# Performance work log

Measured on AMD Instinct MI355X. Metric: run time of the kernel, lower is better.

Reference implementation:

```python
import jax, jax.numpy as jnp
import numpy as np

D_MODEL = 1024
N_HEAD = 16


def setup_inputs() -> dict:
    key = jax.random.key(0)
    ks = jax.random.split(key, 12)
    B, T, D = 2, 2048, D_MODEL
    s = 1.0 / np.sqrt(D)
    return {
        "q": jax.random.normal(ks[0], (B, T, D), jnp.float32),
        "k": jax.random.normal(ks[1], (B, T, D), jnp.float32),
        "v": jax.random.normal(ks[2], (B, T, D), jnp.float32),
        "w_q": jax.random.normal(ks[3], (D, D), jnp.float32) * s,
        "b_q": jnp.zeros((D,), jnp.float32),
        "w_k": jax.random.normal(ks[4], (D, D), jnp.float32) * s,
        "b_k": jnp.zeros((D,), jnp.float32),
        "w_v": jax.random.normal(ks[5], (D, D), jnp.float32) * s,
        "b_v": jnp.zeros((D,), jnp.float32),
        "w_o": jax.random.normal(ks[6], (D, D), jnp.float32) * s,
        "b_o": jnp.zeros((D,), jnp.float32),
    }


def reference(q, k, v, w_q, b_q, w_k, b_k, w_v, b_v, w_o, b_o):
    B, T, D = q.shape
    H = N_HEAD
    nd = D // H  # head dim
    # projections (weights stored as [in, out])
    qh = (q @ w_q + b_q).reshape(B, T, H, nd).transpose(0, 2, 1, 3)  # [b,h,t,nd]
    kh = (k @ w_k + b_k).reshape(B, T, H, nd).transpose(0, 2, 1, 3)
    vh = (v @ w_v + b_v).reshape(B, T, H, nd).transpose(0, 2, 1, 3)
    score = jnp.einsum('bhqd,bhkd->bhqk', qh, kh) / jnp.sqrt(jnp.float32(nd))
    causal = jnp.tril(jnp.ones((T, T), dtype=bool))  # [tq, tk]
    score = jnp.where(causal, score, -jnp.inf)
    # NOTE: original module uses nn.Softmax(dim=-2), i.e. softmax over the
    # QUERY axis. Faithful to the source.
    attn = jax.nn.softmax(score, axis=-2)
    out = jnp.einsum('bhqk,bhkd->bhqd', attn, vh)  # [b,h,t,nd]
    out = out.transpose(0, 2, 1, 3).reshape(B, T, D)
    return out @ w_o + b_o
```

## Files before the change

### kernel.cpp

```cpp
#include <hip/hip_runtime.h>
#include <hip/hip_bf16.h>
#include <cstdint>
#include <cstddef>

#define D_MODEL 1024
#define NHEAD   16
#define HDIM    64
#define BB      2
#define TT      2048
#define MM      (BB*TT)
#define BHN     (BB*NHEAD)

typedef __attribute__((ext_vector_type(8))) __bf16 bf16x8;
typedef __attribute__((ext_vector_type(4))) float  f32x4;
typedef __attribute__((ext_vector_type(8))) unsigned short u16x8;
typedef __attribute__((ext_vector_type(4))) unsigned short u16x4;

__device__ __forceinline__ unsigned short f2b(float f){
  __bf16 b = (__bf16)f;
  return __builtin_bit_cast(unsigned short, b);
}
__device__ __forceinline__ float b2f(unsigned short u){
  unsigned int x = ((unsigned int)u) << 16;
  return __builtin_bit_cast(float, x);
}

__device__ __forceinline__ f32x4 mfma16(bf16x8 a, bf16x8 b, f32x4 c){
  return __builtin_amdgcn_mfma_f32_16x16x32_bf16(a, b, c, 0, 0, 0);
}

__device__ __forceinline__ void gload16(const void* g, void* lds){
  __builtin_amdgcn_global_load_lds((const __attribute__((address_space(1))) void*)g,
                                   (__attribute__((address_space(3))) void*)lds, 16, 0, 0);
}

__global__ void cvt_bf16_kernel(const float* __restrict__ q, const float* __restrict__ k,
                                const float* __restrict__ v,
                                unsigned short* __restrict__ Xq, unsigned short* __restrict__ Xk,
                                unsigned short* __restrict__ Xv){
  const int z = blockIdx.y;
  const float* x = z==0 ? q : z==1 ? k : v;
  unsigned short* y = z==0 ? Xq : z==1 ? Xk : Xv;
  size_t i = (size_t)blockIdx.x*blockDim.x + threadIdx.x;
  const float4* p = (const float4*)(x + i*8);
  float4 a = p[0], b = p[1];
  u16x8 o;
  o[0]=f2b(a.x); o[1]=f2b(a.y); o[2]=f2b(a.z); o[3]=f2b(a.w);
  o[4]=f2b(b.x); o[5]=f2b(b.y); o[6]=f2b(b.z); o[7]=f2b(b.w);
  *(u16x8*)(y + i*8) = o;
}

__global__ void transpose_w_kernel(const float* __restrict__ W0, const float* __restrict__ W1,
                                   const float* __restrict__ W2, const float* __restrict__ W3,
                                   unsigned short* __restrict__ T0, unsigned short* __restrict__ T1,
                                   unsigned short* __restrict__ T2, unsigned short* __restrict__ T3){
  __shared__ float tile[32][33];
  const int z = blockIdx.z;
  const float* W = z==0 ? W0 : z==1 ? W1 : z==2 ? W2 : W3;
  unsigned short* Wt = z==0 ? T0 : z==1 ? T1 : z==2 ? T2 : T3;
  int tx = threadIdx.x, ty = threadIdx.y;
  int x0 = blockIdx.x*32, y0 = blockIdx.y*32;
  #pragma unroll
  for (int i=0;i<4;i++)
    tile[ty + i*8][tx] = W[(size_t)(y0 + ty + i*8)*D_MODEL + x0 + tx];
  __syncthreads();
  #pragma unroll
  for (int i=0;i<4;i++)
    Wt[(size_t)(x0 + ty + i*8)*D_MODEL + y0 + tx] = f2b(tile[tx][ty + i*8]);
}

__device__ __forceinline__ void gemm_body(const unsigned short* __restrict__ A,
                                          const unsigned short* __restrict__ Bt,
                                          const float* __restrict__ bias,
                                          void* __restrict__ Cout, const int mode,
                                          const int m0, const int n0)
{
  constexpr int K = D_MODEL, N = D_MODEL;
  __shared__ unsigned short As[2][128*32];
  __shared__ unsigned short Bs[2][128*32];
  const int t = threadIdx.x, lane = t&63, w = t>>6;
  const int wr = w>>1, wc = w&1, lr = lane&15, lg = lane>>4;
  const int srow = lane>>2;
  const int schunk = (lane&3) ^ ((lane>>3)&3);
  const int crd = lg ^ ((lr>>1)&3);
  f32x4 acc[4][4] = {};

  auto stage = [&](int buf, int k0){
    #pragma unroll
    for (int g=0; g<2; g++){
      int reg = w*2 + g;
      int r = reg*16 + srow;
      gload16(A  + (size_t)(m0+r)*K + k0 + schunk*8, (char*)As[buf] + reg*1024);
      gload16(Bt + (size_t)(n0+r)*K + k0 + schunk*8, (char*)Bs[buf] + reg*1024);
    }
  };

  stage(0, 0);
  __syncthreads();
  int buf = 0;
  for (int ks = 0; ks < 32; ++ks){
    if (ks < 31) stage(buf^1, (ks+1)*32);
    const char* bufA = (const char*)As[buf];
    const char* bufB = (const char*)Bs[buf];
    bf16x8 af[4], bfv[4];
    #pragma unroll
    for (int mi=0;mi<4;mi++){
      int r = wr*64 + mi*16 + lr;
      af[mi] = *(const bf16x8*)(bufA + r*64 + crd*16);
    }
    #pragma unroll
    for (int ni=0;ni<4;ni++){
      int r = wc*64 + ni*16 + lr;
      bfv[ni] = *(const bf16x8*)(bufB + r*64 + crd*16);
    }
    #pragma unroll
    for (int mi=0;mi<4;mi++)
      #pragma unroll
      for (int ni=0;ni<4;ni++)
        acc[mi][ni] = mfma16(af[mi], bfv[ni], acc[mi][ni]);
    __syncthreads();
    buf ^= 1;
  }

  #pragma unroll
  for (int mi=0;mi<4;mi++){
    #pragma unroll
    for (int ni=0;ni<4;ni++){
      int n = n0 + wc*64 + ni*16 + lr;
      int mbase = m0 + wr*64 + mi*16 + lg*4;
      float bv = bias[n];
      if (mode == 0){
        unsigned short* Cb = (unsigned short*)Cout;
        #pragma unroll
        for (int r=0;r<4;r++) Cb[(size_t)(mbase+r)*N + n] = f2b(acc[mi][ni][r] + bv);
      } else {
        unsigned short* Vt = (unsigned short*)Cout;
        int h = n >> 6, d = n & 63;
        int b = mbase >> 11;
        int tq = mbase & (TT-1);
        u16x4 vv;
        #pragma unroll
        for (int r=0;r<4;r++) vv[r] = f2b(acc[mi][ni][r] + bv);
        *(u16x4*)(Vt + ((size_t)((b*NHEAD + h)*HDIM + d))*TT + tq) = vv;
      }
    }
  }
}

__launch_bounds__(256)
__global__ void proj_gemm_kernel(const unsigned short* __restrict__ Xq,
                                 const unsigned short* __restrict__ Xk,
                                 const unsigned short* __restrict__ Xv,
                                 const unsigned short* __restrict__ Wtq,
                                 const unsigned short* __restrict__ Wtk,
                                 const unsigned short* __restrict__ Wtv,
                                 const float* __restrict__ b_q, const float* __restrict__ b_k,
                                 const float* __restrict__ b_v,
                                 unsigned short* __restrict__ Qb, unsigned short* __restrict__ Kb,
                                 unsigned short* __restrict__ Vt)
{
  const int id = blockIdx.x;
  const int xcd = id & 7, r2 = id >> 3;
  const int n = r2 & 7, mz = r2 >> 3;
  const int m = (mz & 3)*8 + xcd, z = mz >> 2;
  const unsigned short* A  = z==0 ? Xq : z==1 ? Xk : Xv;
  const unsigned short* Bt = z==0 ? Wtq : z==1 ? Wtk : Wtv;
  const float* bias = z==0 ? b_q : z==1 ? b_k : b_v;
  void* C = z==0 ? (void*)Qb : z==1 ? (void*)Kb : (void*)Vt;
  gemm_body(A, Bt, bias, C, z==2 ? 1 : 0, m*128, n*128);
}

__launch_bounds__(256)
__global__ void out_gemm_kernel(const unsigned short* __restrict__ Ob,
                                const unsigned short* __restrict__ Wto,
                                const float* __restrict__ b_o, float* __restrict__ out)
{
  constexpr int K = D_MODEL, N = D_MODEL;
  __shared__ unsigned short As[2][64*32];
  __shared__ unsigned short Bs[2][128*32];
  const int id = blockIdx.x;
  const int xcd = id & 7, r2 = id >> 3;
  const int n0 = (r2 & 7)*128, m0 = ((r2 >> 3)*8 + xcd)*64;
  const int t = threadIdx.x, lane = t&63, w = t>>6;
  const int wr = w>>1, wc = w&1, lr = lane&15, lg = lane>>4;
  const int srow = lane>>2;
  const int schunk = (lane&3) ^ ((lane>>3)&3);
  const int crd = lg ^ ((lr>>1)&3);
  f32x4 acc[2][4] = {};

  auto stage = [&](int buf, int k0){
    { int r = w*16 + srow;
      gload16(Ob + (size_t)(m0+r)*K + k0 + schunk*8, (char*)As[buf] + w*1024); }
    #pragma unroll
    for (int g=0; g<2; g++){
      int reg = w*2 + g;
      int r = reg*16 + srow;
      gload16(Wto + (size_t)(n0+r)*K + k0 + schunk*8, (char*)Bs[buf] + reg*1024);
    }
  };

  stage(0, 0);
  __syncthreads();
  int buf = 0;
  for (int ks = 0; ks < 32; ++ks){
    if (ks < 31) stage(buf^1, (ks+1)*32);
    const char* bufA = (const char*)As[buf];
    const char* bufB = (const char*)Bs[buf];
    bf16x8 af[2], bfv[4];
    #pragma unroll
    for (int mi=0;mi<2;mi++){
      int r = wr*32 + mi*16 + lr;
      af[mi] = *(const bf16x8*)(bufA + r*64 + crd*16);
    }
    #pragma unroll
    for (int ni=0;ni<4;ni++){
      int r = wc*64 + ni*16 + lr;
      bfv[ni] = *(const bf16x8*)(bufB + r*64 + crd*16);
    }
    #pragma unroll
    for (int mi=0;mi<2;mi++)
      #pragma unroll
      for (int ni=0;ni<4;ni++)
        acc[mi][ni] = mfma16(af[mi], bfv[ni], acc[mi][ni]);
    __syncthreads();
    buf ^= 1;
  }

  #pragma unroll
  for (int mi=0;mi<2;mi++){
    #pragma unroll
    for (int ni=0;ni<4;ni++){
      int n = n0 + wc*64 + ni*16 + lr;
      int mbase = m0 + wr*32 + mi*16 + lg*4;
      float bv = b_o[n];
      #pragma unroll
      for (int r=0;r<4;r++) out[(size_t)(mbase+r)*N + n] = acc[mi][ni][r] + bv;
    }
  }
}

__launch_bounds__(256)
__global__ void col_stats_kernel(const unsigned short* __restrict__ Qb,
                                 const unsigned short* __restrict__ Kb,
                                 float* __restrict__ partialS)
{
  __shared__ unsigned short Ks[128*64];
  __shared__ unsigned short Qs[2][64*64];
  const int t = threadIdx.x, lane = t&63, w = t>>6;
  const int id = blockIdx.x;
  const int bh = id & 31, pair = id >> 5;
  const int kb_ = pair & 15, qc = pair >> 4;
  const int b = bh >> 4, h = bh & 15;
  const int k0 = kb_ * 128;
  const int lr = lane&15, lg = lane>>4;
  const int osrc = (lane&7) ^ (lane>>3);

  auto stageQ = [&](int buf, int qt){
    #pragma unroll
    for (int g=0; g<2; g++){
      int reg = w*2 + g;
      int r = reg*8 + (lane>>3);
      gload16(Qb + ((size_t)(b*TT + qt + r))*D_MODEL + h*64 + osrc*8,
              (char*)Qs[buf] + reg*1024);
    }
  };

  const int qstart = (k0 > qc*256) ? k0 : qc*256;
  const int qend   = (qc+1)*256;

  #pragma unroll
  for (int g=0; g<4; g++){
    int reg = w*4 + g;
    int r = reg*8 + (lane>>3);
    gload16(Kb + ((size_t)(b*TT + k0 + r))*D_MODEL + h*64 + osrc*8, (char*)Ks + reg*1024);
  }
  if (qstart < qend) stageQ(0, qstart);
  __syncthreads();

  bf16x8 bk[2][2];
  #pragma unroll
  for (int kb=0;kb<2;kb++)
    #pragma unroll
    for (int ks=0;ks<2;ks++){
      int r = w*32 + kb*16 + lr;
      bk[kb][ks] = *(const bf16x8*)((const char*)Ks + r*128 + (((ks*4+lg) ^ (r&7))*16));
    }
  f32x4 sacc[2] = {};
  int buf = 0;
  for (int qt = qstart; qt < qend; qt += 64){
    if (qt + 64 < qend) stageQ(buf^1, qt+64);
    const char* bufQ = (const char*)Qs[buf];
    const bool interior = (qt >= k0 + 128);
    #pragma unroll
    for (int qb=0;qb<4;qb++){
      bf16x8 aq[2];
      #pragma unroll
      for (int ks=0;ks<2;ks++){
        int r = qb*16 + lr;
        aq[ks] = *(const bf16x8*)(bufQ + r*128 + (((ks*4+lg) ^ (r&7))*16));
      }
      f32x4 sf[2] = {};
      #pragma unroll
      for (int ks=0;ks<2;ks++)
        #pragma unroll
        for (int kb=0;kb<2;kb++)
          sf[kb] = mfma16(aq[ks], bk[kb][ks], sf[kb]);
      #pragma unroll
      for (int kb=0;kb<2;kb++){
        int col = k0 + w*32 + kb*16 + lr;
        #pragma unroll
        for (int r=0;r<4;r++){
          float e = __expf(sf[kb][r] * 0.125f);
          if (!interior){
            int qg = qt + qb*16 + lg*4 + r;
            e = (qg >= col) ? e : 0.f;
          }
          sacc[kb][r] += e;
        }
      }
    }
    __syncthreads();
    buf ^= 1;
  }
  #pragma unroll
  for (int kb=0;kb<2;kb++){
    float s = sacc[kb][0] + sacc[kb][1] + sacc[kb][2] + sacc[kb][3];
    s += __shfl_xor(s, 16);
    s += __shfl_xor(s, 32);
    if (lg == 0){
      int col = k0 + w*32 + kb*16 + lr;
      partialS[((size_t)qc*BHN + bh)*TT + col] = s;
    }
  }
}

__global__ void col_combine_kernel(const float* __restrict__ partialS, float* __restrict__ colS){
  int i = blockIdx.x*256 + threadIdx.x;
  float s = 0.f;
  #pragma unroll
  for (int qc=0;qc<8;qc++) s += partialS[(size_t)qc*BHN*TT + i];
  colS[i] = 1.0f / s;
}

__global__ void vscale_kernel(unsigned short* __restrict__ Vt, const float* __restrict__ colS){
  size_t c = (size_t)blockIdx.x*256 + threadIdx.x;
  int t0  = (int)(c & 255) * 8;
  int row = (int)(c >> 8);
  int bh  = row >> 6;
  u16x8 v = *(u16x8*)(Vt + (size_t)row*TT + t0);
  const float4* cs = (const float4*)(colS + (size_t)bh*TT + t0);
  float4 s0 = cs[0], s1 = cs[1];
  v[0]=f2b(b2f(v[0])*s0.x); v[1]=f2b(b2f(v[1])*s0.y);
  v[2]=f2b(b2f(v[2])*s0.z); v[3]=f2b(b2f(v[3])*s0.w);
  v[4]=f2b(b2f(v[4])*s1.x); v[5]=f2b(b2f(v[5])*s1.y);
  v[6]=f2b(b2f(v[6])*s1.z); v[7]=f2b(b2f(v[7])*s1.w);
  *(u16x8*)(Vt + (size_t)row*TT + t0) = v;
}

__launch_bounds__(256)
__global__ void attn_out_kernel(const unsigned short* __restrict__ Qb,
                                const unsigned short* __restrict__ Kb,
                                const unsigned short* __restrict__ Vt,
                                unsigned short* __restrict__ O)
{
  __shared__ unsigned short Qs[64*64];
  __shared__ unsigned short Ks2[2][64*64];
  __shared__ unsigned short Vs[2][64*64];
  __shared__ unsigned short Ps[64*64];
  const int t = threadIdx.x, lane=t&63, w=t>>6;
  const int id = blockIdx.x;
  const int bh = id & 31;
  const int qi = 31 - (id >> 5);
  const int b = bh>>4, h = bh&15;
  const int q0 = qi*64;
  const int lr = lane&15, lg = lane>>4;
  const int osrc = (lane&7) ^ (lane>>3);

  auto stageKV = [&](int buf, int k0){
    #pragma unroll
    for (int g=0; g<2; g++){
      int reg = w*2 + g;
      int r = reg*8 + (lane>>3);
      gload16(Kb + ((size_t)(b*TT + k0 + r))*D_MODEL + h*64 + osrc*8,
              (char*)Ks2[buf] + reg*1024);
      gload16(Vt + ((size_t)(bh*HDIM + r))*TT + k0 + osrc*8,
              (char*)Vs[buf] + reg*1024);
    }
  };

  #pragma unroll
  for (int g=0; g<2; g++){
    int reg = w*2 + g;
    int r = reg*8 + (lane>>3);
    gload16(Qb + ((size_t)(b*TT + q0 + r))*D_MODEL + h*64 + osrc*8, (char*)Qs + reg*1024);
  }
  stageKV(0, 0);
  __syncthreads();

  bf16x8 aq[2];
  #pragma unroll
  for (int ks=0;ks<2;ks++){
    int r = w*16 + lr;
    aq[ks] = *(const bf16x8*)((const char*)Qs + r*128 + (((ks*4+lg) ^ (r&7))*16));
  }
  f32x4 oacc[4] = {};
  const int nkt = qi + 1;
  int buf = 0;
  for (int kt=0; kt<nkt; kt++){
    int k0 = kt*64;
    if (kt+1 < nkt) stageKV(buf^1, k0+64);
    const char* bufK = (const char*)Ks2[buf];
    const char* bufV = (const char*)Vs[buf];
    f32x4 sf[4] = {};
    #pragma unroll
    for (int ks=0;ks<2;ks++)
      #pragma unroll
      for (int kb=0;kb<4;kb++){
        int r = kb*16 + lr;
        bf16x8 bk = *(const bf16x8*)(bufK + r*128 + (((ks*4+lg) ^ (r&7))*16));
        sf[kb] = mfma16(bk, aq[ks], sf[kb]);
      }
    const bool boundary = (kt == qi);
    const int prow = w*16 + lr;
    #pragma unroll
    for (int kb=0;kb<4;kb++){
      u16x4 vv;
      #pragma unroll
      for (int r=0;r<4;r++){
        float pv = __expf(sf[kb][r]*0.125f);
        if (boundary){
          int kg = k0 + kb*16 + lg*4 + r;
          int qg = q0 + prow;
          pv = (qg >= kg) ? pv : 0.f;
        }
        vv[r] = f2b(pv);
      }
      *(u16x4*)((char*)Ps + ((prow*128 + kb*32 + lg*8) ^ ((prow&7)<<4))) = vv;
    }
    #pragma unroll
    for (int ks=0;ks<2;ks++){
      bf16x8 pa = *(const bf16x8*)((const char*)Ps + prow*128 + (((ks*4+lg) ^ (prow&7))*16));
      #pragma unroll
      for (int db=0;db<4;db++){
        int r = db*16 + lr;
        bf16x8 bv = *(const bf16x8*)(bufV + r*128 + (((ks*4+lg) ^ (r&7))*16));
        oacc[db] = mfma16(pa, bv, oacc[db]);
      }
    }
    __syncthreads();
    buf ^= 1;
  }
  #pragma unroll
  for (int db=0;db<4;db++){
    int qg = q0 + w*16 + lg*4;
    int d  = db*16 + lr;
    #pragma unroll
    for (int r=0;r<4;r++)
      O[((size_t)(b*TT + qg + r))*D_MODEL + h*64 + d] = f2b(oacc[db][r]);
  }
}

extern "C" void kernel_launch(void* const* d_in, const int* in_sizes, int n_in,
                              void* d_out, int out_size, void* d_ws, size_t ws_size,
                              hipStream_t stream)
{
  (void)in_sizes; (void)n_in; (void)out_size; (void)ws_size;
  const float* q   = (const float*)d_in[0];
  const float* k   = (const float*)d_in[1];
  const float* v   = (const float*)d_in[2];
  const float* w_q = (const float*)d_in[3];
  const float* b_q = (const float*)d_in[4];
  const float* w_k = (const float*)d_in[5];
  const float* b_k = (const float*)d_in[6];
  const float* w_v = (const float*)d_in[7];
  const float* b_v = (const float*)d_in[8];
  const float* w_o = (const float*)d_in[9];
  const float* b_o = (const float*)d_in[10];

  char* p = (char*)d_ws;
  auto carve = [&](size_t bytes)->char* {
    char* r = p; p += (bytes + 255) & ~(size_t)255; return r;
  };
  unsigned short* Xq  = (unsigned short*)carve((size_t)MM*D_MODEL*2);
  unsigned short* Xk  = (unsigned short*)carve((size_t)MM*D_MODEL*2);
  unsigned short* Xv  = (unsigned short*)carve((size_t)MM*D_MODEL*2);
  unsigned short* Wtq = (unsigned short*)carve((size_t)D_MODEL*D_MODEL*2);
  unsigned short* Wtk = (unsigned short*)carve((size_t)D_MODEL*D_MODEL*2);
  unsigned short* Wtv = (unsigned short*)carve((size_t)D_MODEL*D_MODEL*2);
  unsigned short* Wto = (unsigned short*)carve((size_t)D_MODEL*D_MODEL*2);
  unsigned short* Qb  = (unsigned short*)carve((size_t)MM*D_MODEL*2);
  unsigned short* Kb  = (unsigned short*)carve((size_t)MM*D_MODEL*2);
  unsigned short* Vt  = (unsigned short*)carve((size_t)MM*D_MODEL*2);
  unsigned short* Ob  = (unsigned short*)carve((size_t)MM*D_MODEL*2);
  float* partialS = (float*)carve((size_t)8*BHN*TT*4);
  float* colS     = (float*)carve((size_t)BHN*TT*4);

  cvt_bf16_kernel<<<dim3((MM*D_MODEL/8)/256, 3), 256, 0, stream>>>(q, k, v, Xq, Xk, Xv);

  dim3 tgrid(32,32,4), tblk(32,8);
  transpose_w_kernel<<<tgrid, tblk, 0, stream>>>(w_q, w_k, w_v, w_o, Wtq, Wtk, Wtv, Wto);

  proj_gemm_kernel<<<dim3(768), 256, 0, stream>>>(Xq, Xk, Xv, Wtq, Wtk, Wtv,
                                                  b_q, b_k, b_v, Qb, Kb, Vt);

  col_stats_kernel<<<dim3(8*16*BHN), 256, 0, stream>>>(Qb, Kb, partialS);
  col_combine_kernel<<<dim3(BHN*TT/256), 256, 0, stream>>>(partialS, colS);

  vscale_kernel<<<dim3((BHN*HDIM*TT/8)/256), 256, 0, stream>>>(Vt, colS);

  attn_out_kernel<<<dim3((TT/64)*BHN), 256, 0, stream>>>(Qb, Kb, Vt, Ob);

  out_gemm_kernel<<<dim3(512), 256, 0, stream>>>(Ob, Wto, b_o, (float*)d_out);
}
```

Baseline: 140.7 us.

## Fuse input bf16 conversion into projection GEMM, merge colsum with V scaling, enlarge attention tiles

The projection GEMM now reads fp32 q/k/v directly, converts them to bf16 in registers and writes them to LDS. This removes the separate conversion kernel and its bf16 intermediate buffers. The column-sum combine and the V scaling are merged into one kernel. The attention-output kernel now uses 128-query tiles with 512 threads and per-wave causal skipping plus setprio hints. The A-operand loads go through registers rather than async global-to-LDS copies, which adds register pressure and may hurt load/compute overlap.

```diff
diff --git a/kernel.cpp b/kernel.cpp
--- a/kernel.cpp
+++ b/kernel.cpp
@@ -32,22 +32,6 @@
 __device__ __forceinline__ void gload16(const void* g, void* lds){
   __builtin_amdgcn_global_load_lds((const __attribute__((address_space(1))) void*)g,
                                    (__attribute__((address_space(3))) void*)lds, 16, 0, 0);
-}
-
-__global__ void cvt_bf16_kernel(const float* __restrict__ q, const float* __restrict__ k,
-                                const float* __restrict__ v,
-                                unsigned short* __restrict__ Xq, unsigned short* __restrict__ Xk,
-                                unsigned short* __restrict__ Xv){
-  const int z = blockIdx.y;
-  const float* x = z==0 ? q : z==1 ? k : v;
-  unsigned short* y = z==0 ? Xq : z==1 ? Xk : Xv;
-  size_t i = (size_t)blockIdx.x*blockDim.x + threadIdx.x;
-  const float4* p = (const float4*)(x + i*8);
-  float4 a = p[0], b = p[1];
-  u16x8 o;
-  o[0]=f2b(a.x); o[1]=f2b(a.y); o[2]=f2b(a.z); o[3]=f2b(a.w);
-  o[4]=f2b(b.x); o[5]=f2b(b.y); o[6]=f2b(b.z); o[7]=f2b(b.w);
-  *(u16x8*)(y + i*8) = o;
 }
 
 __global__ void transpose_w_kernel(const float* __restrict__ W0, const float* __restrict__ W1,
@@ -69,11 +53,11 @@
     Wt[(size_t)(x0 + ty + i*8)*D_MODEL + y0 + tx] = f2b(tile[tx][ty + i*8]);
 }
 
-__device__ __forceinline__ void gemm_body(const unsigned short* __restrict__ A,
-                                          const unsigned short* __restrict__ Bt,
-                                          const float* __restrict__ bias,
-                                          void* __restrict__ Cout, const int mode,
-                                          const int m0, const int n0)
+__device__ __forceinline__ void gemm_body_f32A(const float* __restrict__ A,
+                                               const unsigned short* __restrict__ Bt,
+                                               const float* __restrict__ bias,
+                                               void* __restrict__ Cout, const int mode,
+                                               const int m0, const int n0)
 {
   constexpr int K = D_MODEL, N = D_MODEL;
   __shared__ unsigned short As[2][128*32];
@@ -82,24 +66,40 @@
   const int wr = w>>1, wc = w&1, lr = lane&15, lg = lane>>4;
   const int srow = lane>>2;
   const int schunk = (lane&3) ^ ((lane>>3)&3);
+  const int ra = t>>1, half = t&1;
+  const int u0 = (half*2)     ^ ((ra>>1)&3);
+  const int u1 = (half*2 + 1) ^ ((ra>>1)&3);
   const int crd = lg ^ ((lr>>1)&3);
   f32x4 acc[4][4] = {};
-
-  auto stage = [&](int buf, int k0){
+  float4 a0,a1,a2,a3;
+
+  auto loadA = [&](int k0){
+    const float4* pa = (const float4*)(A + (size_t)(m0+ra)*K + k0 + half*16);
+    a0=pa[0]; a1=pa[1]; a2=pa[2]; a3=pa[3];
+  };
+  auto writeA = [&](int buf){
+    u16x8 p0, p1;
+    p0[0]=f2b(a0.x); p0[1]=f2b(a0.y); p0[2]=f2b(a0.z); p0[3]=f2b(a0.w);
+    p0[4]=f2b(a1.x); p0[5]=f2b(a1.y); p0[6]=f2b(a1.z); p0[7]=f2b(a1.w);
+    p1[0]=f2b(a2.x); p1[1]=f2b(a2.y); p1[2]=f2b(a2.z); p1[3]=f2b(a2.w);
+    p1[4]=f2b(a3.x); p1[5]=f2b(a3.y); p1[6]=f2b(a3.z); p1[7]=f2b(a3.w);
+    *(u16x8*)((char*)As[buf] + ra*64 + u0*16) = p0;
+    *(u16x8*)((char*)As[buf] + ra*64 + u1*16) = p1;
+  };
+  auto stageB = [&](int buf, int k0){
     #pragma unroll
     for (int g=0; g<2; g++){
       int reg = w*2 + g;
       int r = reg*16 + srow;
-      gload16(A  + (size_t)(m0+r)*K + k0 + schunk*8, (char*)As[buf] + reg*1024);
       gload16(Bt + (size_t)(n0+r)*K + k0 + schunk*8, (char*)Bs[buf] + reg*1024);
     }
   };
 
-  stage(0, 0);
+  loadA(0); stageB(0, 0); writeA(0);
   __syncthreads();
   int buf = 0;
   for (int ks = 0; ks < 32; ++ks){
-    if (ks < 31) stage(buf^1, (ks+1)*32);
+    if (ks < 31){ loadA((ks+1)*32); stageB(buf^1, (ks+1)*32); }
     const char* bufA = (const char*)As[buf];
     const char* bufB = (const char*)Bs[buf];
     bf16x8 af[4], bfv[4];
@@ -118,6 +118,7 @@
       #pragma unroll
       for (int ni=0;ni<4;ni++)
         acc[mi][ni] = mfma16(af[mi], bfv[ni], acc[mi][ni]);
+    if (ks < 31) writeA(buf^1);
     __syncthreads();
     buf ^= 1;
   }
@@ -148,9 +149,9 @@
 }
 
 __launch_bounds__(256)
-__global__ void proj_gemm_kernel(const unsigned short* __restrict__ Xq,
-                                 const unsigned short* __restrict__ Xk,
-                                 const unsigned short* __restrict__ Xv,
+__global__ void proj_gemm_kernel(const float* __restrict__ q,
+                                 const float* __restrict__ k,
+                                 const float* __restrict__ v,
                                  const unsigned short* __restrict__ Wtq,
                                  const unsigned short* __restrict__ Wtk,
                                  const unsigned short* __restrict__ Wtv,
@@ -163,11 +164,11 @@
   const int xcd = id & 7, r2 = id >> 3;
   const int n = r2 & 7, mz = r2 >> 3;
   const int m = (mz & 3)*8 + xcd, z = mz >> 2;
-  const unsigned short* A  = z==0 ? Xq : z==1 ? Xk : Xv;
+  const float* A  = z==0 ? q : z==1 ? k : v;
   const unsigned short* Bt = z==0 ? Wtq : z==1 ? Wtk : Wtv;
   const float* bias = z==0 ? b_q : z==1 ? b_k : b_v;
   void* C = z==0 ? (void*)Qb : z==1 ? (void*)Kb : (void*)Vt;
-  gemm_body(A, Bt, bias, C, z==2 ? 1 : 0, m*128, n*128);
+  gemm_body_f32A(A, Bt, bias, C, z==2 ? 1 : 0, m*128, n*128);
 }
 
 __launch_bounds__(256)
@@ -334,58 +335,46 @@
   }
 }
 
-__global__ void col_combine_kernel(const float* __restrict__ partialS, float* __restrict__ colS){
-  int i = blockIdx.x*256 + threadIdx.x;
+__global__ void col_combine_vscale_kernel(const float* __restrict__ partialS,
+                                          unsigned short* __restrict__ Vt){
+  const int bh = blockIdx.x >> 3, tc = blockIdx.x & 7;
+  const int col = tc*256 + threadIdx.x;
   float s = 0.f;
   #pragma unroll
-  for (int qc=0;qc<8;qc++) s += partialS[(size_t)qc*BHN*TT + i];
-  colS[i] = 1.0f / s;
-}
-
-__global__ void vscale_kernel(unsigned short* __restrict__ Vt, const float* __restrict__ colS){
-  size_t c = (size_t)blockIdx.x*256 + threadIdx.x;
-  int t0  = (int)(c & 255) * 8;
-  int row = (int)(c >> 8);
-  int bh  = row >> 6;
-  u16x8 v = *(u16x8*)(Vt + (size_t)row*TT + t0);
-  const float4* cs = (const float4*)(colS + (size_t)bh*TT + t0);
-  float4 s0 = cs[0], s1 = cs[1];
-  v[0]=f2b(b2f(v[0])*s0.x); v[1]=f2b(b2f(v[1])*s0.y);
-  v[2]=f2b(b2f(v[2])*s0.z); v[3]=f2b(b2f(v[3])*s0.w);
-  v[4]=f2b(b2f(v[4])*s1.x); v[5]=f2b(b2f(v[5])*s1.y);
-  v[6]=f2b(b2f(v[6])*s1.z); v[7]=f2b(b2f(v[7])*s1.w);
-  *(u16x8*)(Vt + (size_t)row*TT + t0) = v;
-}
-
-__launch_bounds__(256)
+  for (int qc=0;qc<8;qc++) s += partialS[((size_t)qc*BHN + bh)*TT + col];
+  const float inv = 1.0f / s;
+  #pragma unroll 8
+  for (int d=0; d<HDIM; d++){
+    size_t idx = ((size_t)(bh*HDIM + d))*TT + col;
+    Vt[idx] = f2b(b2f(Vt[idx]) * inv);
+  }
+}
+
+__launch_bounds__(512)
 __global__ void attn_out_kernel(const unsigned short* __restrict__ Qb,
                                 const unsigned short* __restrict__ Kb,
                                 const unsigned short* __restrict__ Vt,
                                 unsigned short* __restrict__ O)
 {
-  __shared__ unsigned short Qs[64*64];
+  __shared__ unsigned short Qs[128*64];
   __shared__ unsigned short Ks2[2][64*64];
   __shared__ unsigned short Vs[2][64*64];
-  __shared__ unsigned short Ps[64*64];
+  __shared__ unsigned short Ps[128*64];
   const int t = threadIdx.x, lane=t&63, w=t>>6;
   const int id = blockIdx.x;
   const int bh = id & 31;
-  const int qi = 31 - (id >> 5);
+  const int qi = 15 - (id >> 5);
   const int b = bh>>4, h = bh&15;
-  const int q0 = qi*64;
+  const int q0 = qi*128;
   const int lr = lane&15, lg = lane>>4;
   const int osrc = (lane&7) ^ (lane>>3);
 
   auto stageKV = [&](int buf, int k0){
-    #pragma unroll
-    for (int g=0; g<2; g++){
-      int reg = w*2 + g;
-      int r = reg*8 + (lane>>3);
-      gload16(Kb + ((size_t)(b*TT + k0 + r))*D_MODEL + h*64 + osrc*8,
-              (char*)Ks2[buf] + reg*1024);
-      gload16(Vt + ((size_t)(bh*HDIM + r))*TT + k0 + osrc*8,
-              (char*)Vs[buf] + reg*1024);
-    }
+    int r = w*8 + (lane>>3);
+    gload16(Kb + ((size_t)(b*TT + k0 + r))*D_MODEL + h*64 + osrc*8,
+            (char*)Ks2[buf] + w*1024);
+    gload16(Vt + ((size_t)(bh*HDIM + r))*TT + k0 + osrc*8,
+            (char*)Vs[buf] + w*1024);
   };
 
   #pragma unroll
@@ -404,48 +393,55 @@
     aq[ks] = *(const bf16x8*)((const char*)Qs + r*128 + (((ks*4+lg) ^ (r&7))*16));
   }
   f32x4 oacc[4] = {};
-  const int nkt = qi + 1;
+  const int nkt = 2*qi + 2;
   int buf = 0;
   for (int kt=0; kt<nkt; kt++){
     int k0 = kt*64;
     if (kt+1 < nkt) stageKV(buf^1, k0+64);
-    const char* bufK = (const char*)Ks2[buf];
-    const char* bufV = (const char*)Vs[buf];
-    f32x4 sf[4] = {};
-    #pragma unroll
-    for (int ks=0;ks<2;ks++)
+    const bool active = (k0 <= q0 + w*16 + 15);
+    if (active){
+      const char* bufK = (const char*)Ks2[buf];
+      const char* bufV = (const char*)Vs[buf];
+      f32x4 sf[4] = {};
+      __builtin_amdgcn_s_setprio(1);
+      #pragma unroll
+      for (int ks=0;ks<2;ks++)
+        #pragma unroll
+        for (int kb=0;kb<4;kb++){
+          int r = kb*16 + lr;
+          bf16x8 bk = *(const bf16x8*)(bufK + r*128 + (((ks*4+lg) ^ (r&7))*16));
+          sf[kb] = mfma16(bk, aq[ks], sf[kb]);
+        }
+      __builtin_amdgcn_s_setprio(0);
+      const bool boundary = (k0 + 64 > q0 + w*16);
+      const int prow = w*16 + lr;
       #pragma unroll
       for (int kb=0;kb<4;kb++){
-        int r = kb*16 + lr;
-        bf16x8 bk = *(const bf16x8*)(bufK + r*128 + (((ks*4+lg) ^ (r&7))*16));
-        sf[kb] = mfma16(bk, aq[ks], sf[kb]);
+        u16x4 vv;
+        #pragma unroll
+        for (int r=0;r<4;r++){
+          float pv = __expf(sf[kb][r]*0.125f);
+          if (boundary){
+            int kg = k0 + kb*16 + lg*4 + r;
+            int qg = q0 + prow;
+            pv = (qg >= kg) ? pv : 0.f;
+          }
+          vv[r] = f2b(pv);
+        }
+        *(u16x4*)((char*)Ps + ((prow*128 + kb*32 + lg*8) ^ ((prow&7)<<4))) = vv;
       }
-    const bool boundary = (kt == qi);
-    const int prow = w*16 + lr;
-    #pragma unroll
-    for (int kb=0;kb<4;kb++){
-      u16x4 vv;
-      #pragma unroll
-      for (int r=0;r<4;r++){
-        float pv = __expf(sf[kb][r]*0.125f);
-        if (boundary){
-          int kg = k0 + kb*16 + lg*4 + r;
-          int qg = q0 + prow;
-          pv = (qg >= kg) ? pv : 0.f;
+      __builtin_amdgcn_s_setprio(1);
+      #pragma unroll
+      for (int ks=0;ks<2;ks++){
+        bf16x8 pa = *(const bf16x8*)((const char*)Ps + prow*128 + (((ks*4+lg) ^ (prow&7))*16));
+        #pragma unroll
+        for (int db=0;db<4;db++){
+          int r = db*16 + lr;
+          bf16x8 bv = *(const bf16x8*)(bufV + r*128 + (((ks*4+lg) ^ (r&7))*16));
+          oacc[db] = mfma16(pa, bv, oacc[db]);
         }
-        vv[r] = f2b(pv);
       }
-      *(u16x4*)((char*)Ps + ((prow*128 + kb*32 + lg*8) ^ ((prow&7)<<4))) = vv;
-    }
-    #pragma unroll
-    for (int ks=0;ks<2;ks++){
-      bf16x8 pa = *(const bf16x8*)((const char*)Ps + prow*128 + (((ks*4+lg) ^ (prow&7))*16));
-      #pragma unroll
-      for (int db=0;db<4;db++){
-        int r = db*16 + lr;
-        bf16x8 bv = *(const bf16x8*)(bufV + r*128 + (((ks*4+lg) ^ (r&7))*16));
-        oacc[db] = mfma16(pa, bv, oacc[db]);
-      }
+      __builtin_amdgcn_s_setprio(0);
     }
     __syncthreads();
     buf ^= 1;
@@ -481,9 +477,6 @@
   auto carve = [&](size_t bytes)->char* {
     char* r = p; p += (bytes + 255) & ~(size_t)255; return r;
   };
-  unsigned short* Xq  = (unsigned short*)carve((size_t)MM*D_MODEL*2);
-  unsigned short* Xk  = (unsigned short*)carve((size_t)MM*D_MODEL*2);
-  unsigned short* Xv  = (unsigned short*)carve((size_t)MM*D_MODEL*2);
   unsigned short* Wtq = (unsigned short*)carve((size_t)D_MODEL*D_MODEL*2);
   unsigned short* Wtk = (unsigned short*)carve((size_t)D_MODEL*D_MODEL*2);
   unsigned short* Wtv = (unsigned short*)carve((size_t)D_MODEL*D_MODEL*2);
@@ -493,22 +486,17 @@
   unsigned short* Vt  = (unsigned short*)carve((size_t)MM*D_MODEL*2);
   unsigned short* Ob  = (unsigned short*)carve((size_t)MM*D_MODEL*2);
   float* partialS = (float*)carve((size_t)8*BHN*TT*4);
-  float* colS     = (float*)carve((size_t)BHN*TT*4);
-
-  cvt_bf16_kernel<<<dim3((MM*D_MODEL/8)/256, 3), 256, 0, stream>>>(q, k, v, Xq, Xk, Xv);
 
   dim3 tgrid(32,32,4), tblk(32,8);
   transpose_w_kernel<<<tgrid, tblk, 0, stream>>>(w_q, w_k, w_v, w_o, Wtq, Wtk, Wtv, Wto);
 
-  proj_gemm_kernel<<<dim3(768), 256, 0, stream>>>(Xq, Xk, Xv, Wtq, Wtk, Wtv,
+  proj_gemm_kernel<<<dim3(768), 256, 0, stream>>>(q, k, v, Wtq, Wtk, Wtv,
                                                   b_q, b_k, b_v, Qb, Kb, Vt);
 
   col_stats_kernel<<<dim3(8*16*BHN), 256, 0, stream>>>(Qb, Kb, partialS);
-  col_combine_kernel<<<dim3(BHN*TT/256), 256, 0, stream>>>(partialS, colS);
-
-  vscale_kernel<<<dim3((BHN*HDIM*TT/8)/256), 256, 0, stream>>>(Vt, colS);
-
-  attn_out_kernel<<<dim3((TT/64)*BHN), 256, 0, stream>>>(Qb, Kb, Vt, Ob);
+  col_combine_vscale_kernel<<<dim3(BHN*8), 256, 0, stream>>>(partialS, Vt);
+
+  attn_out_kernel<<<dim3((TT/128)*BHN), 512, 0, stream>>>(Qb, Kb, Vt, Ob);
 
   out_gemm_kernel<<<dim3(512), 256, 0, stream>>>(Ob, Wto, b_o, (float*)d_out);
 }
```

New measurement: 151.7 us. 1.08x slower.
